# Performance work log

Hardware: AMD Instinct MI355X
Metric: run time of the kernel (lower is better)

## Reference

```python
import jax, jax.numpy as jnp
import numpy as np

N_QUBITS = 8
PI = float(np.pi)
C64 = jnp.complex64


def _apply_1q(state, U, w):
    # state: [B] + [2]*N_QUBITS, U: [2,2] complex. Contract qubit axis w.
    ax = 1 + w
    s = jnp.moveaxis(state, ax, -1)
    s = jnp.einsum('...j,ij->...i', s, U)
    return jnp.moveaxis(s, -1, ax)


def _apply_cx(state, c, t):
    # CNOT with control wire c, target wire t: flip target where control=1.
    axc, axt = 1 + c, 1 + t
    s = jnp.moveaxis(state, axc, 1)
    axt_new = axt + 1 if axt < axc else axt
    flipped = jnp.flip(s[:, 1], axis=axt_new - 1)
    s = jnp.stack([s[:, 0], flipped], axis=1)
    return jnp.moveaxis(s, 1, axc)


def _rz(t):
    em = jnp.exp(-0.5j * t)
    ep = jnp.exp(0.5j * t)
    z = jnp.zeros((), C64)
    return jnp.stack([jnp.stack([em, z]), jnp.stack([z, ep])]).astype(C64)


def _ry(t):
    c, s = jnp.cos(0.5 * t), jnp.sin(0.5 * t)
    return jnp.stack([jnp.stack([c, -s]), jnp.stack([s, c])]).astype(C64)


def _u3(t, p, l):
    ct, st = jnp.cos(0.5 * t), jnp.sin(0.5 * t)
    one = jnp.ones((), C64)
    r0 = jnp.stack([ct * one, -jnp.exp(1j * l) * st])
    r1 = jnp.stack([jnp.exp(1j * p) * st, jnp.exp(1j * (p + l)) * ct])
    return jnp.stack([r0, r1]).astype(C64)


def _expval_z(state, w):
    p = state.real ** 2 + state.imag ** 2
    p = jnp.moveaxis(p, 1 + w, 1)
    B = p.shape[0]
    p = p.reshape(B, 2, -1)
    return p[:, 0].sum(-1) - p[:, 1].sum(-1)


def _forward(x, conv_rz, conv_ry, conv_ry2, pool, W1, b1, W2, b2):
    B = x.shape[0]
    # angle-encoding circuit: RY(x_i) on each wire from |0...0> -> product state
    state = jnp.ones((B, 1), C64)
    for w in range(N_QUBITS):
        q = jnp.stack([jnp.cos(0.5 * x[:, w]), jnp.sin(0.5 * x[:, w])], axis=-1).astype(C64)
        state = (state[:, :, None] * q[:, None, :]).reshape(B, -1)
    state = state.reshape((B,) + (2,) * N_QUBITS)

    rz_m = _rz(jnp.float32(-PI / 2))
    rz_p = _rz(jnp.float32(PI / 2))
    n_layers = int(np.log2(N_QUBITS)) - 1  # = 2
    active = list(range(N_QUBITS))
    cc = pc = 0
    for _layer in range(n_layers):
        pairs = [(active[i], active[i + 1]) for i in range(len(active)) if i % 2 == 0 and i < len(active) - 1]
        pairs += [(active[i], active[i + 1]) for i in range(len(active)) if i % 2 == 1 and i < len(active) - 1]
        for (q0, q1) in pairs:
            state = _apply_1q(state, rz_m, q1)
            state = _apply_cx(state, q1, q0)
            state = _apply_1q(state, _rz(conv_rz[cc]), q0)
            state = _apply_1q(state, _ry(conv_ry[cc]), q1)
            state = _apply_cx(state, q0, q1)
            state = _apply_1q(state, _ry(conv_ry2[cc]), q1)
            state = _apply_cx(state, q1, q0)
            state = _apply_1q(state, rz_p, q0)
            cc += 1
        remain = [q for i, q in enumerate(active) if i % 2 == 1]
        # mid-circuit expvals on meas qubits are discarded in the source -> no-op
        for q in remain:
            state = _apply_1q(state, _u3(pool[pc, 0], pool[pc, 1], pool[pc, 2]), q)
            pc += 1
        active = remain

    feats = jnp.stack([_expval_z(state, w) for w in active], axis=-1)  # [B, 2]
    h = jnp.tanh(feats @ W1.T + b1)
    out = h @ W2.T + b2
    return jax.nn.sigmoid(out)


def setup_inputs() -> dict:
    key = jax.random.key(0)
    ks = jax.random.split(key, 10)
    B = 65536
    x = jax.random.uniform(ks[0], (B, N_QUBITS), jnp.float32)
    conv_rz = jax.random.uniform(ks[1], (12,), jnp.float32, 0.0, 2 * PI)
    conv_ry = jax.random.uniform(ks[2], (12,), jnp.float32, 0.0, 2 * PI)
    conv_ry2 = jax.random.uniform(ks[3], (12,), jnp.float32, 0.0, 2 * PI)
    pool = jax.random.uniform(ks[4], (6, 3), jnp.float32, 0.0, 2 * PI)
    W1 = jax.random.normal(ks[5], (10, 2), jnp.float32) * 0.5
    b1 = jnp.zeros((10,), jnp.float32)
    W2 = jax.random.normal(ks[6], (1, 10), jnp.float32) * 0.3
    b2 = jnp.zeros((1,), jnp.float32)
    return {"x": x, "conv_rz": conv_rz, "conv_ry": conv_ry, "conv_ry2": conv_ry2,
            "pool": pool, "W1": W1, "b1": b1, "W2": W2, "b2": b2}


def reference(x, conv_rz, conv_ry, conv_ry2, pool, W1, b1, W2, b2):
    return _forward(x, conv_rz, conv_ry, conv_ry2, pool, W1, b1, W2, b2)
```

## Files before the change

### kernel.cpp

```cpp
#include <hip/hip_runtime.h>
#include <math.h>


__device__ __align__(16) float g_T[17496];

struct c32 { float x, y; };
__device__ __forceinline__ c32 cmul(c32 a, c32 b){ return c32{a.x*b.x - a.y*b.y, a.x*b.y + a.y*b.x}; }
__device__ __forceinline__ c32 cadd(c32 a, c32 b){ return c32{a.x+b.x, a.y+b.y}; }
__device__ __forceinline__ c32 csel(bool c, c32 a, c32 b){ return c32{c?a.x:b.x, c?a.y:b.y}; }

struct PP { float a, b, c, d; };

__device__ __forceinline__ float pget(int i, PP pp) {
    float s = (i < 64) ? pp.a : (i < 128) ? pp.b : (i < 192) ? pp.c : pp.d;
    return __uint_as_float(__builtin_amdgcn_readlane(__float_as_uint(s), i & 63));
}
#define P(I) pget((I), pp)

template<int M>
__device__ __forceinline__ float sx(float v) {
    if constexpr (M == 1) {
        return __int_as_float(__builtin_amdgcn_update_dpp(
            __float_as_int(v), __float_as_int(v), 0xB1, 0xF, 0xF, false));
    } else if constexpr (M == 2) {
        return __int_as_float(__builtin_amdgcn_update_dpp(
            __float_as_int(v), __float_as_int(v), 0x4E, 0xF, 0xF, false));
    } else if constexpr (M == 4) {
        return __int_as_float(__builtin_amdgcn_ds_swizzle(__float_as_int(v), 0x101F));
    } else {
        return __int_as_float(__builtin_amdgcn_ds_swizzle(__float_as_int(v), 0x201F));
    }
}

template<int RM, int LQ, bool KEEPD, int BASE>
__device__ __forceinline__ void conv_A(c32 s[16], int sub, PP pp) {
    #pragma unroll
    for (int r = 0; r < 16; ++r) if (r & RM) { s[r].x = sx<LQ>(s[r].x); s[r].y = sx<LQ>(s[r].y); }
    const bool cb = (sub & LQ) != 0;
    const c32 M00 = csel(cb, c32{P(BASE+8),P(BASE+9)},   c32{P(BASE+0),P(BASE+1)});
    const c32 M01 = csel(cb, c32{P(BASE+10),P(BASE+11)}, c32{P(BASE+2),P(BASE+3)});
    const c32 M10 = csel(cb, c32{P(BASE+12),P(BASE+13)}, c32{P(BASE+4),P(BASE+5)});
    const c32 M11 = csel(cb, c32{P(BASE+14),P(BASE+15)}, c32{P(BASE+6),P(BASE+7)});
    #pragma unroll
    for (int r = 0; r < 16; ++r) if (!(r & RM)) {
        c32 lo = s[r], hi = s[r|RM];
        s[r]    = cadd(cmul(M00,lo), cmul(M01,hi));
        s[r|RM] = cadd(cmul(M10,lo), cmul(M11,hi));
    }
    if constexpr (KEEPD) {
        #pragma unroll
        for (int r = 0; r < 16; ++r) if (r & RM) { s[r].x = sx<LQ>(s[r].x); s[r].y = sx<LQ>(s[r].y); }
    }
}

template<int RM, int LQ, int BASE>
__device__ __forceinline__ void conv_B(c32 s[16], int sub, PP pp) {
    const bool cb = (sub & LQ) != 0;
    #pragma unroll
    for (int r = 0; r < 16; ++r) if (!(r & RM)) {
        c32 lo = s[r], hi = s[r|RM];
        s[r]    = csel(cb, hi, lo);
        s[r|RM] = csel(cb, lo, hi);
    }
    const c32 RS0 = csel(cb, c32{P(BASE+6),P(BASE+7)},   c32{P(BASE+0),P(BASE+1)});
    const c32 RP0 = csel(cb, c32{P(BASE+4),P(BASE+5)},   c32{P(BASE+2),P(BASE+3)});
    const c32 RS1 = csel(cb, c32{P(BASE+14),P(BASE+15)}, c32{P(BASE+8),P(BASE+9)});
    const c32 RP1 = csel(cb, c32{P(BASE+12),P(BASE+13)}, c32{P(BASE+10),P(BASE+11)});
    #pragma unroll
    for (int r = 0; r < 16; ++r) {
        c32 pt{ sx<LQ>(s[r].x), sx<LQ>(s[r].y) };
        const c32 RS = (r & RM) ? RS1 : RS0;
        const c32 RP = (r & RM) ? RP1 : RP0;
        s[r] = cadd(cmul(RS, s[r]), cmul(RP, pt));
    }
}

template<int CM, int TM, bool KEEPD, int BASE>
__device__ __forceinline__ void conv_RR(c32 s[16], PP pp) {
    c32 m[2][2][2];
    #pragma unroll
    for (int q = 0; q < 2; ++q)
      #pragma unroll
      for (int i = 0; i < 2; ++i)
        #pragma unroll
        for (int j = 0; j < 2; ++j)
          m[q][i][j] = c32{ P(BASE + q*8 + i*4 + j*2), P(BASE + q*8 + i*4 + j*2 + 1) };
    #pragma unroll
    for (int r = 0; r < 16; ++r) if ((r & TM) && !(r & CM)) { c32 t = s[r]; s[r] = s[r|CM]; s[r|CM] = t; }
    #pragma unroll
    for (int r = 0; r < 16; ++r) if (!(r & TM)) {
        const int q = (r & CM) ? 1 : 0;
        c32 lo = s[r], hi = s[r|TM];
        s[r]    = cadd(cmul(m[q][0][0],lo), cmul(m[q][0][1],hi));
        s[r|TM] = cadd(cmul(m[q][1][0],lo), cmul(m[q][1][1],hi));
    }
    if constexpr (KEEPD) {
        #pragma unroll
        for (int r = 0; r < 16; ++r) if ((r & TM) && !(r & CM)) { c32 t = s[r]; s[r] = s[r|CM]; s[r|CM] = t; }
    }
}

template<int RM, int BASE>
__device__ __forceinline__ void pool_plain(c32 s[16], PP pp) {
    const c32 V00{P(BASE+0),P(BASE+1)}, V01{P(BASE+2),P(BASE+3)};
    const c32 V10{P(BASE+4),P(BASE+5)}, V11{P(BASE+6),P(BASE+7)};
    #pragma unroll
    for (int r = 0; r < 16; ++r) if (!(r & RM)) {
        c32 lo = s[r], hi = s[r|RM];
        s[r]    = cadd(cmul(V00,lo), cmul(V01,hi));
        s[r|RM] = cadd(cmul(V10,lo), cmul(V11,hi));
    }
}
template<int RM, int LQ, int BASE>
__device__ __forceinline__ void pool_lanec(c32 s[16], int sub, PP pp) {
    const bool cb = (sub & LQ) != 0;
    const c32 E00 = csel(cb, c32{P(BASE+2),P(BASE+3)}, c32{P(BASE+0),P(BASE+1)});
    const c32 E01 = csel(cb, c32{P(BASE+0),P(BASE+1)}, c32{P(BASE+2),P(BASE+3)});
    const c32 E10 = csel(cb, c32{P(BASE+6),P(BASE+7)}, c32{P(BASE+4),P(BASE+5)});
    const c32 E11 = csel(cb, c32{P(BASE+4),P(BASE+5)}, c32{P(BASE+6),P(BASE+7)});
    #pragma unroll
    for (int r = 0; r < 16; ++r) if (!(r & RM)) {
        c32 lo = s[r], hi = s[r|RM];
        s[r]    = cadd(cmul(E00,lo), cmul(E01,hi));
        s[r|RM] = cadd(cmul(E10,lo), cmul(E11,hi));
    }
}
template<int RM, int CRM, int BASE>
__device__ __forceinline__ void pool_regc(c32 s[16], PP pp) {
    const c32 V00{P(BASE+0),P(BASE+1)}, V01{P(BASE+2),P(BASE+3)};
    const c32 V10{P(BASE+4),P(BASE+5)}, V11{P(BASE+6),P(BASE+7)};
    #pragma unroll
    for (int r = 0; r < 16; ++r) if (!(r & RM)) {
        const bool swp = (r & CRM) != 0;
        const c32 A = swp ? V01 : V00, Bm = swp ? V00 : V01;
        const c32 C = swp ? V11 : V10, D  = swp ? V10 : V11;
        c32 lo = s[r], hi = s[r|RM];
        s[r]    = cadd(cmul(A,lo),  cmul(Bm,hi));
        s[r|RM] = cadd(cmul(C,lo),  cmul(D,hi));
    }
}

__device__ __forceinline__ float tanh_fast(float x) {
    float e = __expf(2.f * x);
    return (e - 1.f) / (e + 1.f);
}

__launch_bounds__(256)
__global__ void qcnn_eval_grid(const float* __restrict__ rz,  const float* __restrict__ ry,
                               const float* __restrict__ ry2, const float* __restrict__ pool) {
    __shared__ float par[256];
    const int tid = threadIdx.x;

    if (tid < 10) {
        const int cc = tid;
        const bool hasD = (cc <= 3) || (cc == 7) || (cc == 8);
        float tz = rz[cc], ta = ry[cc], tb = ry2[cc];
        float cz = __cosf(0.5f*tz), szz = __sinf(0.5f*tz);
        float cp = __cosf(0.5f*(ta+tb)), sp = __sinf(0.5f*(ta+tb));
        float cm = __cosf(0.5f*(ta-tb)), sm = __sinf(0.5f*(ta-tb));
        float A0[2][2] = {{cp,-sp},{sp,cp}};
        float A1[2][2] = {{sm,cm},{cm,-sm}};
        float* o = par + 16*cc;
        #pragma unroll
        for (int which = 0; which < 2; ++which) {
            float px = cz, py = which ? szz : -szz;
            #pragma unroll
            for (int row = 0; row < 2; ++row)
              #pragma unroll
              for (int col = 0; col < 2; ++col) {
                float ex = which ? A1[row][col] : A0[row][col], ey = 0.f;
                if (hasD && col == 1) { ey = -ex; ex = 0.f; }
                o[which*8 + row*4 + col*2 + 0] = px*ex - py*ey;
                o[which*8 + row*4 + col*2 + 1] = px*ey + py*ex;
            }
        }
    } else if (tid < 16) {
        const int pc = tid - 10;
        const bool hasS = (pc <= 2) || (pc == 4);
        float th = pool[3*pc], ph = pool[3*pc+1], la = pool[3*pc+2];
        float ct = __cosf(0.5f*th), st = __sinf(0.5f*th);
        float u[2][2][2] = {
            {{ct, 0.f},                    {-__cosf(la)*st, -__sinf(la)*st}},
            {{__cosf(ph)*st, __sinf(ph)*st}, {__cosf(ph+la)*ct, __sinf(ph+la)*ct}}};
        if (hasS) {
            #pragma unroll
            for (int row = 0; row < 2; ++row) {
                float xx = u[row][1][0], yy = u[row][1][1];
                u[row][1][0] = -yy; u[row][1][1] = xx;
            }
        }
        float* o = par + 160 + 8*pc;
        #pragma unroll
        for (int row = 0; row < 2; ++row)
          #pragma unroll
          for (int col = 0; col < 2; ++col) {
            o[row*4+col*2+0] = u[row][col][0];
            o[row*4+col*2+1] = u[row][col][1];
        }
    } else if (tid < 64) {
        par[208 + (tid - 16)] = 0.f;
    }
    __syncthreads();

    const int lane = tid & 63;
    const int sub  = lane & 15;
    PP pp{ par[lane], par[lane+64], par[lane+128], par[lane+192] };
    const int gwave = (blockIdx.x * blockDim.x + tid) >> 6;
    const int b = gwave * 4 + (lane >> 4);

    const float H = 0.8660254037844386f;
    float cw[8], sw_[8];
    int rr = b;
    #pragma unroll
    for (int w = 0; w < 8; ++w) {
        int t = rr % 3; rr /= 3;
        cw[w]  = (t == 0) ? 1.f : 0.5f;
        sw_[w] = (t == 0) ? 0.f : ((t == 1) ? H : -H);
    }

    float a = ((sub & 8) ? sw_[0] : cw[0]);
    a *= (sub & 1) ? sw_[2] : cw[2];
    a *= (sub & 2) ? sw_[4] : cw[4];
    a *= (sub & 4) ? sw_[6] : cw[6];

    c32 s[16];
    float a13[4] = {cw[1]*cw[3], sw_[1]*cw[3], cw[1]*sw_[3], sw_[1]*sw_[3]};
    float a57[4] = {cw[5]*cw[7], sw_[5]*cw[7], cw[5]*sw_[7], sw_[5]*sw_[7]};
    #pragma unroll
    for (int r = 0; r < 16; ++r) s[r] = c32{ a * a13[r & 3] * a57[r >> 2], 0.f };

    conv_A<1, 8, false,  0>(s, sub, pp);
    conv_A<2, 1, true,  16>(s, sub, pp);
    conv_A<4, 2, true,  32>(s, sub, pp);
    conv_A<8, 4, true,  48>(s, sub, pp);
    conv_B<1, 1, 64>(s, sub, pp);
    conv_B<2, 2, 80>(s, sub, pp);
    conv_B<4, 4, 96>(s, sub, pp);
    pool_lanec<1, 1, 160>(s, sub, pp);
    pool_lanec<2, 2, 168>(s, sub, pp);
    pool_lanec<4, 4, 176>(s, sub, pp);
    pool_plain<8, 184>(s, pp);
    conv_RR<1, 2, false, 112>(s, pp);
    conv_RR<4, 8, true,  128>(s, pp);
    conv_RR<2, 4, false, 144>(s, pp);
    pool_regc<2, 4, 192>(s, pp);
    pool_plain<8, 200>(s, pp);

    float e3 = 0.f, e7 = 0.f;
    #pragma unroll
    for (int r = 0; r < 16; ++r) {
        float p = s[r].x*s[r].x + s[r].y*s[r].y;
        e3 += (r & 2) ? -p : p;
        e7 += (r & 8) ? -p : p;
    }
    e3 += sx<1>(e3); e3 += sx<2>(e3); e3 += sx<4>(e3); e3 += sx<8>(e3);
    e7 += sx<1>(e7); e7 += sx<2>(e7); e7 += sx<4>(e7); e7 += sx<8>(e7);

    if (sub == 0 && b < 6561) {
        int j = b % 81, k = b / 81;
        int aa = k % 9, bq = k / 9;
        int base = j * 108 + bq * 12 + aa;
        g_T[base]        = e3;
        g_T[8748 + base] = e7;
    }
}

template<int B0, int B1>
__device__ __forceinline__ void row_dot(const float* __restrict__ Trow,
                                        const float (&p)[4][9], const float (&q)[4][9],
                                        float (&y)[4]) {
    #pragma unroll
    for (int b = B0; b < B1; ++b) {
        const float4 T0 = *reinterpret_cast<const float4*>(Trow + b*12);
        const float4 T1 = *reinterpret_cast<const float4*>(Trow + b*12 + 4);
        const float  T8 = Trow[b*12 + 8];
        #pragma unroll
        for (int e = 0; e < 4; ++e) {
            float sacc = T0.x * p[e][0];
            sacc = fmaf(T0.y, p[e][1], sacc);
            sacc = fmaf(T0.z, p[e][2], sacc);
            sacc = fmaf(T0.w, p[e][3], sacc);
            sacc = fmaf(T1.x, p[e][4], sacc);
            sacc = fmaf(T1.y, p[e][5], sacc);
            sacc = fmaf(T1.z, p[e][6], sacc);
            sacc = fmaf(T1.w, p[e][7], sacc);
            sacc = fmaf(T8,   p[e][8], sacc);
            y[e] = fmaf(q[e][b], sacc, y[e]);
        }
    }
}

__device__ __forceinline__ void lag3(float xv, float& l0, float& l1, float& l2) {
    const float  A = 0.33333333333333333f;
    const float  K = 0.57735026918962576f;
    float c = __cosf(xv), s = __sinf(xv);
    l0 = fmaf(2.f * A, c, A);
    float m = A * (1.f - c);
    l1 = fmaf(K, s, m);
    l2 = fmaf(-K, s, m);
}

__launch_bounds__(768, 3)
__global__ void qcnn_apply(const float* __restrict__ x,
                           const float* __restrict__ W1, const float* __restrict__ b1,
                           const float* __restrict__ W2, const float* __restrict__ b2,
                           float* __restrict__ out, int B) {
    __shared__ __align__(16) float Tl[17496 + 12*64*4];
    float* Pl = Tl + 17496;
    {
        float4* Td = reinterpret_cast<float4*>(Tl);
        const float4* Ts = reinterpret_cast<const float4*>(g_T);
        for (int i = threadIdx.x; i < 4374; i += 768) Td[i] = Ts[i];
    }

    const int tid  = threadIdx.x;
    const int lane = tid & 63;
    const int wave = tid >> 6;
    const int tt   = wave & 1;
    const int rest = wave >> 1;
    const int t3   = rest % 3;
    const int bh   = rest / 3;

    const int gbase = (blockIdx.x * 64 + lane) * 4;

    float p[4][9], q[4][9], g10[4][9];
    float g3v[4], L20[4], L21[4], L22[4];
    #pragma unroll
    for (int e = 0; e < 4; ++e) {
        int idx = gbase + e; if (idx >= B) idx = B - 1;
        const float4 xa = *reinterpret_cast<const float4*>(x + idx*8);
        const float4 xb = *reinterpret_cast<const float4*>(x + idx*8 + 4);
        float l0[3], l1[3], l2[3], l3[3], l4[3], l5[3], l6[3], l7[3];
        lag3(xa.x, l0[0], l0[1], l0[2]);
        lag3(xa.y, l1[0], l1[1], l1[2]);
        lag3(xa.z, l2[0], l2[1], l2[2]);
        lag3(xa.w, l3[0], l3[1], l3[2]);
        lag3(xb.x, l4[0], l4[1], l4[2]);
        lag3(xb.y, l5[0], l5[1], l5[2]);
        lag3(xb.z, l6[0], l6[1], l6[2]);
        lag3(xb.w, l7[0], l7[1], l7[2]);
        #pragma unroll
        for (int u = 0; u < 3; ++u)
          #pragma unroll
          for (int v = 0; v < 3; ++v) {
            g10[e][u + 3*v] = l0[u] * l1[v];
            p[e][u + 3*v]   = l4[u] * l5[v];
            q[e][u + 3*v]   = l6[u] * l7[v];
        }
        g3v[e] = (t3 == 0) ? l3[0] : ((t3 == 1) ? l3[1] : l3[2]);
        L20[e] = l2[0]; L21[e] = l2[1]; L22[e] = l2[2];
    }

    __syncthreads();

    float acc[4] = {0.f, 0.f, 0.f, 0.f};
    const float* Tt = Tl + tt * 8748 + t3 * 27 * 108;
    for (int t2 = 0; t2 < 3; ++t2) {
        float u23[4];
        #pragma unroll
        for (int e = 0; e < 4; ++e) {
            float g2 = (t2 == 0) ? L20[e] : ((t2 == 1) ? L21[e] : L22[e]);
            u23[e] = g3v[e] * g2;
        }
        const float* rb = Tt + t2 * 9 * 108;
        #pragma unroll
        for (int jj = 0; jj < 9; ++jj) {
            float y[4] = {0.f, 0.f, 0.f, 0.f};
            if (bh == 0) row_dot<0, 4>(rb + jj*108, p, q, y);
            else         row_dot<4, 9>(rb + jj*108, p, q, y);
            #pragma unroll
            for (int e = 0; e < 4; ++e)
                acc[e] = fmaf(u23[e] * g10[e][jj], y[e], acc[e]);
        }
    }

    #pragma unroll
    for (int e = 0; e < 4; ++e) Pl[wave*256 + lane*4 + e] = acc[e];
    __syncthreads();

    if (tid < 256) {
        const int elem = blockIdx.x * 256 + tid;
        if (elem < B) {
            float e3 = 0.f, e7 = 0.f;
            #pragma unroll
            for (int r = 0; r < 6; ++r) {
                e3 += Pl[(2*r)   * 256 + tid];
                e7 += Pl[(2*r+1) * 256 + tid];
            }
            float z = b2[0];
            #pragma unroll
            for (int i = 0; i < 10; ++i) {
                float h = tanh_fast(W1[2*i]*e3 + W1[2*i+1]*e7 + b1[i]);
                z += W2[i]*h;
            }
            out[elem] = 1.f / (1.f + __expf(-z));
        }
    }
}

extern "C" void kernel_launch(void* const* d_in, const int* in_sizes, int n_in,
                              void* d_out, int out_size, void* d_ws, size_t ws_size,
                              hipStream_t stream) {
    const float* x       = (const float*)d_in[0];
    const float* conv_rz = (const float*)d_in[1];
    const float* conv_ry = (const float*)d_in[2];
    const float* conv_ry2= (const float*)d_in[3];
    const float* pool    = (const float*)d_in[4];
    const float* W1      = (const float*)d_in[5];
    const float* b1      = (const float*)d_in[6];
    const float* W2      = (const float*)d_in[7];
    const float* b2      = (const float*)d_in[8];
    float* out = (float*)d_out;
    (void)d_ws; (void)ws_size;

    int B = in_sizes[0] / 8;

    qcnn_eval_grid<<<411, 256, 0, stream>>>(conv_rz, conv_ry, conv_ry2, pool);
    qcnn_apply<<<(B + 255) / 256, 768, 0, stream>>>(x, W1, b1, W2, b2, out, B);
}
```

Baseline: 56.70 us.

## Read transfer tensor directly from global memory with repacked layout, drop LDS staging

Drops the per-block copy of the 17.5K-float coefficient table into shared memory and its barrier. Waves now read the table straight from global memory with wave-uniform bases, which should become scalar or cached loads. The table is repacked so each 9-wide row splits into an 8-float aligned part plus a separate 9th-column array, removing padding and letting the leftover column come in one vector load. It also alternates which half of the rows each wave pair handles per t2 step and fully unrolls the t2 loop. The cost is that every wave hits L1/L2 for table data instead of LDS, which depends on cache hit rates and scalar load throughput.

After: 46.64 us. -17.7%, faster.

```diff
diff --git a/kernel.cpp b/kernel.cpp
--- a/kernel.cpp
+++ b/kernel.cpp
@@ -2,7 +2,7 @@
 #include <math.h>
 
 
-__device__ __align__(16) float g_T[17496];
+__device__ __align__(16) float g_T[13608];
 
 struct c32 { float x, y; };
 __device__ __forceinline__ c32 cmul(c32 a, c32 b){ return c32{a.x*b.x - a.y*b.y, a.x*b.y + a.y*b.x}; }
@@ -180,7 +180,7 @@
         float th = pool[3*pc], ph = pool[3*pc+1], la = pool[3*pc+2];
         float ct = __cosf(0.5f*th), st = __sinf(0.5f*th);
         float u[2][2][2] = {
-            {{ct, 0.f},                    {-__cosf(la)*st, -__sinf(la)*st}},
+            {{ct, 0.f},                      {-__cosf(la)*st, -__sinf(la)*st}},
             {{__cosf(ph)*st, __sinf(ph)*st}, {__cosf(ph+la)*ct, __sinf(ph+la)*ct}}};
         if (hasS) {
             #pragma unroll
@@ -259,21 +259,37 @@
     if (sub == 0 && b < 6561) {
         int j = b % 81, k = b / 81;
         int aa = k % 9, bq = k / 9;
-        int base = j * 108 + bq * 12 + aa;
-        g_T[base]        = e3;
-        g_T[8748 + base] = e7;
+        if (aa < 8) {
+            int base = j * 72 + bq * 8 + aa;
+            g_T[base]        = e3;
+            g_T[5832 + base] = e7;
+        } else {
+            int base = 11664 + j * 12 + bq;
+            g_T[base]       = e3;
+            g_T[972 + base] = e7;
+        }
     }
 }
 
 template<int B0, int B1>
 __device__ __forceinline__ void row_dot(const float* __restrict__ Trow,
+                                        const float* __restrict__ T8row,
                                         const float (&p)[4][9], const float (&q)[4][9],
                                         float (&y)[4]) {
+    float t8v[B1 - B0];
+    if constexpr (B0 == 0) {
+        const float4 t = *reinterpret_cast<const float4*>(T8row);
+        t8v[0] = t.x; t8v[1] = t.y; t8v[2] = t.z; t8v[3] = t.w;
+    } else {
+        const float4 t = *reinterpret_cast<const float4*>(T8row + 4);
+        t8v[0] = t.x; t8v[1] = t.y; t8v[2] = t.z; t8v[3] = t.w;
+        t8v[4] = T8row[8];
+    }
     #pragma unroll
     for (int b = B0; b < B1; ++b) {
-        const float4 T0 = *reinterpret_cast<const float4*>(Trow + b*12);
-        const float4 T1 = *reinterpret_cast<const float4*>(Trow + b*12 + 4);
-        const float  T8 = Trow[b*12 + 8];
+        const float4 T0 = *reinterpret_cast<const float4*>(Trow + b*8);
+        const float4 T1 = *reinterpret_cast<const float4*>(Trow + b*8 + 4);
+        const float  t8 = t8v[b - B0];
         #pragma unroll
         for (int e = 0; e < 4; ++e) {
             float sacc = T0.x * p[e][0];
@@ -284,15 +300,15 @@
             sacc = fmaf(T1.y, p[e][5], sacc);
             sacc = fmaf(T1.z, p[e][6], sacc);
             sacc = fmaf(T1.w, p[e][7], sacc);
-            sacc = fmaf(T8,   p[e][8], sacc);
+            sacc = fmaf(t8,   p[e][8], sacc);
             y[e] = fmaf(q[e][b], sacc, y[e]);
         }
     }
 }
 
 __device__ __forceinline__ void lag3(float xv, float& l0, float& l1, float& l2) {
-    const float  A = 0.33333333333333333f;
-    const float  K = 0.57735026918962576f;
+    const float A = 0.33333333333333333f;
+    const float K = 0.57735026918962576f;
     float c = __cosf(xv), s = __sinf(xv);
     l0 = fmaf(2.f * A, c, A);
     float m = A * (1.f - c);
@@ -305,13 +321,7 @@
                            const float* __restrict__ W1, const float* __restrict__ b1,
                            const float* __restrict__ W2, const float* __restrict__ b2,
                            float* __restrict__ out, int B) {
-    __shared__ __align__(16) float Tl[17496 + 12*64*4];
-    float* Pl = Tl + 17496;
-    {
-        float4* Td = reinterpret_cast<float4*>(Tl);
-        const float4* Ts = reinterpret_cast<const float4*>(g_T);
-        for (int i = threadIdx.x; i < 4374; i += 768) Td[i] = Ts[i];
-    }
+    __shared__ float Pl[3072];
 
     const int tid  = threadIdx.x;
     const int lane = tid & 63;
@@ -351,10 +361,11 @@
         L20[e] = l2[0]; L21[e] = l2[1]; L22[e] = l2[2];
     }
 
-    __syncthreads();
+    const int tmBase = __builtin_amdgcn_readfirstlane(tt * 5832 + t3 * 1944);
+    const int t8Base = __builtin_amdgcn_readfirstlane(11664 + tt * 972 + t3 * 324);
 
     float acc[4] = {0.f, 0.f, 0.f, 0.f};
-    const float* Tt = Tl + tt * 8748 + t3 * 27 * 108;
+    #pragma unroll
     for (int t2 = 0; t2 < 3; ++t2) {
         float u23[4];
         #pragma unroll
@@ -362,12 +373,14 @@
             float g2 = (t2 == 0) ? L20[e] : ((t2 == 1) ? L21[e] : L22[e]);
             u23[e] = g3v[e] * g2;
         }
-        const float* rb = Tt + t2 * 9 * 108;
+        const float* Tt2  = g_T + tmBase + t2 * 648;
+        const float* T8t2 = g_T + t8Base + t2 * 108;
+        const bool takeLow = (bh == 0) ^ (t2 == 1);
         #pragma unroll
         for (int jj = 0; jj < 9; ++jj) {
             float y[4] = {0.f, 0.f, 0.f, 0.f};
-            if (bh == 0) row_dot<0, 4>(rb + jj*108, p, q, y);
-            else         row_dot<4, 9>(rb + jj*108, p, q, y);
+            if (takeLow) row_dot<0, 4>(Tt2 + jj*72, T8t2 + jj*12, p, q, y);
+            else         row_dot<4, 9>(Tt2 + jj*72, T8t2 + jj*12, p, q, y);
             #pragma unroll
             for (int e = 0; e < 4; ++e)
                 acc[e] = fmaf(u23[e] * g10[e][jj], y[e], acc[e]);
```

## Hold coefficient tensor in registers per wave and broadcast via readlane

Applied to the files above, without the earlier changes.

The precompute kernel now writes the coefficient tensor in a per-role packed layout, split into 12 slices of 1152 floats with the bh work split balanced across t2. Each wave loads its slice into 18 VGPRs per lane, and the apply kernel broadcasts values with readlane instead of reading them from LDS. This removes the 70 KB LDS staging copy, its __syncthreads and the LDS reads, which should allow more occupancy. In exchange the inner loop issues one readlane per coefficient (scalar broadcast) and uses more registers.

Measured after the change: 71.48 us. +26.1%, slower.

```diff
diff --git a/kernel.cpp b/kernel.cpp
--- a/kernel.cpp
+++ b/kernel.cpp
@@ -2,7 +2,7 @@
 #include <math.h>
 
 
-__device__ __align__(16) float g_T[17496];
+__device__ float g_R[13824];
 
 struct c32 { float x, y; };
 __device__ __forceinline__ c32 cmul(c32 a, c32 b){ return c32{a.x*b.x - a.y*b.y, a.x*b.y + a.y*b.x}; }
@@ -180,7 +180,7 @@
         float th = pool[3*pc], ph = pool[3*pc+1], la = pool[3*pc+2];
         float ct = __cosf(0.5f*th), st = __sinf(0.5f*th);
         float u[2][2][2] = {
-            {{ct, 0.f},                    {-__cosf(la)*st, -__sinf(la)*st}},
+            {{ct, 0.f},                      {-__cosf(la)*st, -__sinf(la)*st}},
             {{__cosf(ph)*st, __sinf(ph)*st}, {__cosf(ph+la)*ct, __sinf(ph+la)*ct}}};
         if (hasS) {
             #pragma unroll
@@ -257,42 +257,28 @@
     e7 += sx<1>(e7); e7 += sx<2>(e7); e7 += sx<4>(e7); e7 += sx<8>(e7);
 
     if (sub == 0 && b < 6561) {
-        int j = b % 81, k = b / 81;
-        int aa = k % 9, bq = k / 9;
-        int base = j * 108 + bq * 12 + aa;
-        g_T[base]        = e3;
-        g_T[8748 + base] = e7;
-    }
-}
-
-template<int B0, int B1>
-__device__ __forceinline__ void row_dot(const float* __restrict__ Trow,
-                                        const float (&p)[4][9], const float (&q)[4][9],
-                                        float (&y)[4]) {
-    #pragma unroll
-    for (int b = B0; b < B1; ++b) {
-        const float4 T0 = *reinterpret_cast<const float4*>(Trow + b*12);
-        const float4 T1 = *reinterpret_cast<const float4*>(Trow + b*12 + 4);
-        const float  T8 = Trow[b*12 + 8];
-        #pragma unroll
-        for (int e = 0; e < 4; ++e) {
-            float sacc = T0.x * p[e][0];
-            sacc = fmaf(T0.y, p[e][1], sacc);
-            sacc = fmaf(T0.z, p[e][2], sacc);
-            sacc = fmaf(T0.w, p[e][3], sacc);
-            sacc = fmaf(T1.x, p[e][4], sacc);
-            sacc = fmaf(T1.y, p[e][5], sacc);
-            sacc = fmaf(T1.z, p[e][6], sacc);
-            sacc = fmaf(T1.w, p[e][7], sacc);
-            sacc = fmaf(T8,   p[e][8], sacc);
-            y[e] = fmaf(q[e][b], sacc, y[e]);
-        }
+        int jj = b % 9;
+        int t2 = (b / 9) % 3;
+        int t3 = (b / 27) % 3;
+        int k  = b / 81;
+        int aa = k % 9;
+        int bq = k / 9;
+        int bh = (bq < 4) ? ((t2 == 1) ? 1 : 0) : ((t2 == 1) ? 0 : 1);
+        int c0 = (bh == 0) ? 4 : 5;
+        int c1 = (bh == 0) ? 5 : 4;
+        int c2 = (bh == 0) ? 4 : 5;
+        int baseRows = (t2 == 0) ? 0 : ((t2 == 1) ? 9*c0 : 9*(c0+c1));
+        int cnt = (t2 == 0) ? c0 : ((t2 == 1) ? c1 : c2);
+        int bqIdx = (bq < 4) ? bq : bq - 4;
+        int pos = (baseRows + jj*cnt + bqIdx)*9 + aa;
+        g_R[(t3*2 + bh)*1152 + pos]       = e3;
+        g_R[(6 + t3*2 + bh)*1152 + pos]   = e7;
     }
 }
 
 __device__ __forceinline__ void lag3(float xv, float& l0, float& l1, float& l2) {
-    const float  A = 0.33333333333333333f;
-    const float  K = 0.57735026918962576f;
+    const float A = 0.33333333333333333f;
+    const float K = 0.57735026918962576f;
     float c = __cosf(xv), s = __sinf(xv);
     l0 = fmaf(2.f * A, c, A);
     float m = A * (1.f - c);
@@ -300,18 +286,50 @@
     l2 = fmaf(-K, s, m);
 }
 
+template<int BH>
+__device__ __forceinline__ void contract(const float (&tr)[18],
+                                         const float (&p)[4][9], const float (&q)[4][9],
+                                         const float (&g10)[4][9],
+                                         const float (&u23)[3][4],
+                                         float (&acc)[4]) {
+    constexpr int cnts[3] = { (BH==0)?4:5, (BH==0)?5:4, (BH==0)?4:5 };
+    int base = 0;
+    #pragma unroll
+    for (int t2 = 0; t2 < 3; ++t2) {
+        const int cnt = cnts[t2];
+        const int lo  = ((BH==0) ^ (t2==1)) ? 0 : 4;
+        #pragma unroll
+        for (int jj = 0; jj < 9; ++jj) {
+            float y[4] = {0.f, 0.f, 0.f, 0.f};
+            #pragma unroll
+            for (int bi = 0; bi < cnt; ++bi) {
+                const int row = base + jj*cnt + bi;
+                float sv[4] = {0.f, 0.f, 0.f, 0.f};
+                #pragma unroll
+                for (int a = 0; a < 9; ++a) {
+                    const int pos = row*9 + a;
+                    const float tv = __uint_as_float(__builtin_amdgcn_readlane(
+                        __float_as_uint(tr[pos >> 6]), pos & 63));
+                    #pragma unroll
+                    for (int e = 0; e < 4; ++e) sv[e] = fmaf(tv, p[e][a], sv[e]);
+                }
+                #pragma unroll
+                for (int e = 0; e < 4; ++e) y[e] = fmaf(q[e][lo + bi], sv[e], y[e]);
+            }
+            #pragma unroll
+            for (int e = 0; e < 4; ++e)
+                acc[e] = fmaf(u23[t2][e] * g10[e][jj], y[e], acc[e]);
+        }
+        base += 9 * cnt;
+    }
+}
+
 __launch_bounds__(768, 3)
 __global__ void qcnn_apply(const float* __restrict__ x,
                            const float* __restrict__ W1, const float* __restrict__ b1,
                            const float* __restrict__ W2, const float* __restrict__ b2,
                            float* __restrict__ out, int B) {
-    __shared__ __align__(16) float Tl[17496 + 12*64*4];
-    float* Pl = Tl + 17496;
-    {
-        float4* Td = reinterpret_cast<float4*>(Tl);
-        const float4* Ts = reinterpret_cast<const float4*>(g_T);
-        for (int i = threadIdx.x; i < 4374; i += 768) Td[i] = Ts[i];
-    }
+    __shared__ float Pl[3072];
 
     const int tid  = threadIdx.x;
     const int lane = tid & 63;
@@ -320,11 +338,17 @@
     const int rest = wave >> 1;
     const int t3   = rest % 3;
     const int bh   = rest / 3;
+    const int roleId = tt*6 + t3*2 + bh;
+
+    float tr[18];
+    #pragma unroll
+    for (int kk = 0; kk < 18; ++kk)
+        tr[kk] = g_R[roleId*1152 + kk*64 + lane];
 
     const int gbase = (blockIdx.x * 64 + lane) * 4;
 
     float p[4][9], q[4][9], g10[4][9];
-    float g3v[4], L20[4], L21[4], L22[4];
+    float u23[3][4];
     #pragma unroll
     for (int e = 0; e < 4; ++e) {
         int idx = gbase + e; if (idx >= B) idx = B - 1;
@@ -347,32 +371,15 @@
             p[e][u + 3*v]   = l4[u] * l5[v];
             q[e][u + 3*v]   = l6[u] * l7[v];
         }
-        g3v[e] = (t3 == 0) ? l3[0] : ((t3 == 1) ? l3[1] : l3[2]);
-        L20[e] = l2[0]; L21[e] = l2[1]; L22[e] = l2[2];
-    }
-
-    __syncthreads();
+        const float g3 = (t3 == 0) ? l3[0] : ((t3 == 1) ? l3[1] : l3[2]);
+        u23[0][e] = g3 * l2[0];
+        u23[1][e] = g3 * l2[1];
+        u23[2][e] = g3 * l2[2];
+    }
 
     float acc[4] = {0.f, 0.f, 0.f, 0.f};
-    const float* Tt = Tl + tt * 8748 + t3 * 27 * 108;
-    for (int t2 = 0; t2 < 3; ++t2) {
-        float u23[4];
-        #pragma unroll
-        for (int e = 0; e < 4; ++e) {
-            float g2 = (t2 == 0) ? L20[e] : ((t2 == 1) ? L21[e] : L22[e]);
-            u23[e] = g3v[e] * g2;
-        }
-        const float* rb = Tt + t2 * 9 * 108;
-        #pragma unroll
-        for (int jj = 0; jj < 9; ++jj) {
-            float y[4] = {0.f, 0.f, 0.f, 0.f};
-            if (bh == 0) row_dot<0, 4>(rb + jj*108, p, q, y);
-            else         row_dot<4, 9>(rb + jj*108, p, q, y);
-            #pragma unroll
-            for (int e = 0; e < 4; ++e)
-                acc[e] = fmaf(u23[e] * g10[e][jj], y[e], acc[e]);
-        }
-    }
+    if (bh == 0) contract<0>(tr, p, q, g10, u23, acc);
+    else         contract<1>(tr, p, q, g10, u23, acc);
 
     #pragma unroll
     for (int e = 0; e < 4; ++e) Pl[wave*256 + lane*4 + e] = acc[e];
```
